# Optimization experiments

Measured on AMD Instinct MI355X. Metric: run time of the kernel, lower is better.

The kernel has to match this reference:

```python
import jax, jax.numpy as jnp
import numpy as np
import math

D_MODEL, D_K, D_V = 1024, 64, 64
B, S = 4, 4096


def setup_inputs() -> dict:
    key = jax.random.key(0)
    ks = jax.random.split(key, 7)
    lim = 1.0 / math.sqrt(D_MODEL)
    return {
        "embeddings": jax.random.normal(ks[0], (B, S, D_MODEL), dtype=jnp.float32),
        "Wq": jax.random.uniform(ks[1], (D_MODEL, D_K), minval=-lim, maxval=lim, dtype=jnp.float32),
        "bq": jax.random.uniform(ks[2], (D_K,), minval=-lim, maxval=lim, dtype=jnp.float32),
        "Wk": jax.random.uniform(ks[3], (D_MODEL, D_K), minval=-lim, maxval=lim, dtype=jnp.float32),
        "bk": jax.random.uniform(ks[4], (D_K,), minval=-lim, maxval=lim, dtype=jnp.float32),
        "Wv": jax.random.uniform(ks[5], (D_MODEL, D_V), minval=-lim, maxval=lim, dtype=jnp.float32),
        "bv": jax.random.uniform(ks[6], (D_V,), minval=-lim, maxval=lim, dtype=jnp.float32),
    }


def reference(embeddings, Wq, bq, Wk, bk, Wv, bv):
    # Q, K: [B, S, d_k]; V: [B, S, d_v]
    Q = embeddings @ Wq + bq
    K = embeddings @ Wk + bk
    V = embeddings @ Wv + bv
    scale = 1.0 / math.sqrt(D_K)
    # scores: [B, S, S]
    scores = jnp.einsum("bsk,btk->bst", Q, K) * scale
    attn = jax.nn.softmax(scores, axis=-1)
    return jnp.einsum("bst,btv->bsv", attn, V)
```

## Files before the change

### kernel.cpp

```cpp
#include <hip/hip_runtime.h>

#define SEQ  4096
#define DMODEL 1024
#define QTOT 16384
#define QSCALE 0.18033688011112042f

typedef __bf16 bf16x8 __attribute__((ext_vector_type(8)));
typedef unsigned short u16x8 __attribute__((ext_vector_type(8)));
typedef float f32x4 __attribute__((ext_vector_type(4)));

static __device__ __forceinline__ unsigned short f2bfbits(float f) {
    unsigned int u = __builtin_bit_cast(unsigned int, f);
    unsigned int lsb = (u >> 16) & 1u;
    u += 0x7fffu + lsb;
    return (unsigned short)(u >> 16);
}

static __device__ __forceinline__ bf16x8 ld_frag(const unsigned short* p) {
    uint4 u = *reinterpret_cast<const uint4*>(p);
    return __builtin_bit_cast(bf16x8, u);
}

__global__ void prep_weights(const float* __restrict__ Wq,
                             const float* __restrict__ Wk,
                             const float* __restrict__ Wv,
                             unsigned short* __restrict__ WtS) {
    int o = blockIdx.x * 256 + threadIdx.x;
    int f = o >> 9, q = o & 511;
    int lane = q >> 3, j = q & 7;
    int kc = f / 12, nt = f - kc * 12;
    int n = nt * 16 + (lane & 15);
    int k = kc * 32 + (lane >> 4) * 8 + j;
    float v;
    if (n < 64)       v = Wq[k * 64 + n];
    else if (n < 128) v = Wk[k * 64 + (n - 64)];
    else              v = Wv[k * 64 + (n - 128)];
    WtS[o] = f2bfbits(v);
}

__global__ __launch_bounds__(256) void proj_cs(
        const float* __restrict__ emb, const unsigned short* __restrict__ WtS,
        const float* __restrict__ bq, const float* __restrict__ bk,
        const float* __restrict__ bv,
        unsigned short* __restrict__ Qb, unsigned short* __restrict__ Kb,
        unsigned short* __restrict__ VT) {
    __shared__ __align__(16) unsigned short Et[2][32 * 256];

    const int tid = threadIdx.x;
    const int w = tid >> 6, lane = tid & 63;
    const int c = lane & 15, qd = lane >> 4;
    const int m = w & 1, nh = w >> 1;
    const int mbase = blockIdx.x * 32;

    f32x4 acc[6];
#pragma unroll
    for (int i = 0; i < 6; i++) acc[i] = (f32x4){0.f, 0.f, 0.f, 0.f};

    const unsigned short* wpB = WtS + nh * 3072 + lane * 8;

    {
        float4 g[8];
#pragma unroll
        for (int rr = 0; rr < 8; rr++)
            g[rr] = *reinterpret_cast<const float4*>(
                emb + (size_t)(mbase + w * 8 + rr) * DMODEL + lane * 4);
#pragma unroll
        for (int rr = 0; rr < 8; rr++) {
            int row = w * 8 + rr;
            ushort4 p;
            p.x = f2bfbits(g[rr].x); p.y = f2bfbits(g[rr].y);
            p.z = f2bfbits(g[rr].z); p.w = f2bfbits(g[rr].w);
            int off = (lane * 8) ^ ((row & 7) << 4);
            *reinterpret_cast<ushort4*>(
                reinterpret_cast<char*>(&Et[0][0]) + row * 512 + off) = p;
        }
    }

    bf16x8 wc[6];
#pragma unroll
    for (int jj = 0; jj < 6; jj++) wc[jj] = ld_frag(wpB + jj * 512);

    __syncthreads();

    int cur = 0;
    for (int mega = 0; mega < 4; mega++) {
        float4 g[8];
        if (mega < 3) {
#pragma unroll
            for (int rr = 0; rr < 8; rr++)
                g[rr] = *reinterpret_cast<const float4*>(
                    emb + (size_t)(mbase + w * 8 + rr) * DMODEL
                        + (mega + 1) * 256 + lane * 4);
        }

        const char* Eb = reinterpret_cast<const char*>(&Et[cur][0]);
        bf16x8 aq[8];
#pragma unroll
        for (int ks = 0; ks < 8; ks++) {
            int off = (ks * 64 + qd * 16) ^ ((c & 7) << 4);
            aq[ks] = ld_frag(reinterpret_cast<const unsigned short*>(
                Eb + (m * 16 + c) * 512 + off));
        }

#pragma unroll
        for (int ks = 0; ks < 8; ks++) {
            int s = mega * 8 + ks;
            bf16x8 wn[6];
            if (s < 31) {
#pragma unroll
                for (int jj = 0; jj < 6; jj++)
                    wn[jj] = ld_frag(wpB + (s + 1) * 6144 + jj * 512);
            } else {
#pragma unroll
                for (int jj = 0; jj < 6; jj++) wn[jj] = wc[jj];
            }
#pragma unroll
            for (int jj = 0; jj < 6; jj++)
                acc[jj] = __builtin_amdgcn_mfma_f32_16x16x32_bf16(aq[ks], wc[jj], acc[jj], 0, 0, 0);
#pragma unroll
            for (int jj = 0; jj < 6; jj++) wc[jj] = wn[jj];
        }

        if (mega < 3) {
#pragma unroll
            for (int rr = 0; rr < 8; rr++) {
                int row = w * 8 + rr;
                ushort4 p;
                p.x = f2bfbits(g[rr].x); p.y = f2bfbits(g[rr].y);
                p.z = f2bfbits(g[rr].z); p.w = f2bfbits(g[rr].w);
                int off = (lane * 8) ^ ((row & 7) << 4);
                *reinterpret_cast<ushort4*>(
                    reinterpret_cast<char*>(&Et[cur ^ 1][0]) + row * 512 + off) = p;
            }
        }
        __syncthreads();
        cur ^= 1;
    }

#pragma unroll
    for (int jj = 0; jj < 6; jj++) {
        int n = (nh * 6 + jj) * 16 + c;
        float bias = (n < 64) ? bq[n] : (n < 128) ? bk[n - 64] : bv[n - 128];
        float fac = (n < 64) ? QSCALE : 1.0f;
#pragma unroll
        for (int r = 0; r < 4; r++) {
            int token = mbase + m * 16 + qd * 4 + r;
            unsigned short bits = f2bfbits((acc[jj][r] + bias) * fac);
            if (n < 64)        Qb[(size_t)token * 64 + n] = bits;
            else if (n < 128)  Kb[(size_t)token * 64 + (n - 64)] = bits;
            else {
                int bb = token >> 12, ss = token & 4095;
                VT[((size_t)bb * 64 + (n - 128)) * SEQ + ss] = bits;
            }
        }
    }
}

__global__ __launch_bounds__(512, 2) void attn(
        const unsigned short* __restrict__ Qb, const unsigned short* __restrict__ Kb,
        const unsigned short* __restrict__ VT,
        float* __restrict__ accP, float* __restrict__ lsumP) {
    __shared__ __align__(16) unsigned short Pl[8][64 * 72];
    __shared__ float l_all[8][64];

    const int tid = threadIdx.x;
    const int w = tid >> 6, lane = tid & 63;
    const int c = lane & 15, qd = lane >> 4;
    const int g3 = blockIdx.x & 7;
    const int b = g3 >> 1;
    const int th = g3 & 1;
    const int qblk = blockIdx.x >> 3;
    const int qbase = qblk * 64;
    const int tstart = th * 2048 + w * 256;

    bf16x8 aq0[4], aq1[4];
#pragma unroll
    for (int qs = 0; qs < 4; qs++) {
        const unsigned short* Qp = Qb + ((size_t)(b << 12) + qbase + qs * 16 + c) * 64 + qd * 8;
        aq0[qs] = ld_frag(Qp);
        aq1[qs] = ld_frag(Qp + 32);
    }

    f32x4 acc[16];
#pragma unroll
    for (int i = 0; i < 16; i++) acc[i] = (f32x4){0.f, 0.f, 0.f, 0.f};
    float lsum[4][4];
#pragma unroll
    for (int qs = 0; qs < 4; qs++)
#pragma unroll
        for (int r = 0; r < 4; r++) lsum[qs][r] = 0.f;

    unsigned short* myP = &Pl[w][0];

#pragma unroll 2
    for (int it = 0; it < 4; it++) {
        const int t0 = tstart + it * 64;
        const unsigned short* Kt = Kb + ((size_t)(b << 12) + t0) * 64;

        bf16x8 bk0[4], bk1[4];
#pragma unroll
        for (int ts = 0; ts < 4; ts++) {
            bk0[ts] = ld_frag(Kt + (ts * 16 + c) * 64 + qd * 8);
            bk1[ts] = ld_frag(Kt + (ts * 16 + c) * 64 + 32 + qd * 8);
        }

#pragma unroll
        for (int qs = 0; qs < 4; qs++) {
            f32x4 sc[4];
#pragma unroll
            for (int ts = 0; ts < 4; ts++) {
                f32x4 z = (f32x4){0.f, 0.f, 0.f, 0.f};
                z = __builtin_amdgcn_mfma_f32_16x16x32_bf16(aq0[qs], bk0[ts], z, 0, 0, 0);
                z = __builtin_amdgcn_mfma_f32_16x16x32_bf16(aq1[qs], bk1[ts], z, 0, 0, 0);
                sc[ts] = z;
            }
#pragma unroll
            for (int ts = 0; ts < 4; ts++)
#pragma unroll
                for (int r = 0; r < 4; r++) {
                    float p = __builtin_amdgcn_exp2f(sc[ts][r]);
                    lsum[qs][r] += p;
                    myP[(qs * 16 + qd * 4 + r) * 72 + ts * 16 + c] = f2bfbits(p);
                }
        }

        bf16x8 bv0[4], bv1[4];
#pragma unroll
        for (int nt = 0; nt < 4; nt++) {
            const unsigned short* Vp = VT + (((size_t)b * 64 + nt * 16 + c) << 12) + t0 + qd * 8;
            bv0[nt] = ld_frag(Vp);
            bv1[nt] = ld_frag(Vp + 32);
        }

#pragma unroll
        for (int qs = 0; qs < 4; qs++) {
            bf16x8 ap0 = ld_frag(&myP[(qs * 16 + c) * 72 + qd * 8]);
            bf16x8 ap1 = ld_frag(&myP[(qs * 16 + c) * 72 + 32 + qd * 8]);
#pragma unroll
            for (int nt = 0; nt < 4; nt++) {
                acc[qs * 4 + nt] = __builtin_amdgcn_mfma_f32_16x16x32_bf16(ap0, bv0[nt], acc[qs * 4 + nt], 0, 0, 0);
                acc[qs * 4 + nt] = __builtin_amdgcn_mfma_f32_16x16x32_bf16(ap1, bv1[nt], acc[qs * 4 + nt], 0, 0, 0);
            }
        }
    }

#pragma unroll
    for (int off = 1; off < 16; off <<= 1)
#pragma unroll
        for (int qs = 0; qs < 4; qs++)
#pragma unroll
            for (int r = 0; r < 4; r++) lsum[qs][r] += __shfl_xor(lsum[qs][r], off);
    if (c == 0) {
#pragma unroll
        for (int qs = 0; qs < 4; qs++)
#pragma unroll
            for (int r = 0; r < 4; r++)
                l_all[w][qs * 16 + qd * 4 + r] = lsum[qs][r];
    }

    float* red = (float*)&Pl[0][0];
    __syncthreads();
    if (w >= 4) {
        float* rp = red + (w - 4) * 4352 + lane * 68;
#pragma unroll
        for (int i = 0; i < 16; i++) *reinterpret_cast<f32x4*>(rp + i * 4) = acc[i];
    }
    __syncthreads();
    if (w < 4) {
        float* rp = red + w * 4352 + lane * 68;
#pragma unroll
        for (int i = 0; i < 16; i++) acc[i] += *reinterpret_cast<const f32x4*>(rp + i * 4);
    }
    __syncthreads();
    if (w == 2 || w == 3) {
        float* rp = red + (w - 2) * 4352 + lane * 68;
#pragma unroll
        for (int i = 0; i < 16; i++) *reinterpret_cast<f32x4*>(rp + i * 4) = acc[i];
    }
    __syncthreads();
    if (w < 2) {
        float* rp = red + w * 4352 + lane * 68;
#pragma unroll
        for (int i = 0; i < 16; i++) acc[i] += *reinterpret_cast<const f32x4*>(rp + i * 4);
    }
    __syncthreads();
    if (w == 1) {
        float* rp = red + lane * 68;
#pragma unroll
        for (int i = 0; i < 16; i++) *reinterpret_cast<f32x4*>(rp + i * 4) = acc[i];
    }
    __syncthreads();
    if (w == 0) {
        float* rp = red + lane * 68;
#pragma unroll
        for (int i = 0; i < 16; i++) acc[i] += *reinterpret_cast<const f32x4*>(rp + i * 4);
        float* accOut = accP + (size_t)th * ((size_t)QTOT * 64);
        float* lOut   = lsumP + (size_t)th * QTOT;
#pragma unroll
        for (int qs = 0; qs < 4; qs++)
#pragma unroll
            for (int r = 0; r < 4; r++) {
                int q = qs * 16 + qd * 4 + r;
                float l = 0.f;
#pragma unroll
                for (int ww = 0; ww < 8; ww++) l += l_all[ww][q];
                size_t row = (size_t)(b << 12) + qbase + q;
                lOut[row] = l;
#pragma unroll
                for (int nt = 0; nt < 4; nt++)
                    accOut[row * 64 + nt * 16 + c] = acc[qs * 4 + nt][r];
            }
    }
}

__global__ __launch_bounds__(256) void finalize(
        const float* __restrict__ accP, const float* __restrict__ lsumP,
        float* __restrict__ out) {
    int idx = blockIdx.x * 256 + threadIdx.x;
    int row = idx >> 4;
    float4 a0 = reinterpret_cast<const float4*>(accP)[idx];
    float4 a1 = reinterpret_cast<const float4*>(accP)[idx + QTOT * 16];
    float inv = 1.0f / (lsumP[row] + lsumP[row + QTOT]);
    float4 o;
    o.x = (a0.x + a1.x) * inv;
    o.y = (a0.y + a1.y) * inv;
    o.z = (a0.z + a1.z) * inv;
    o.w = (a0.w + a1.w) * inv;
    reinterpret_cast<float4*>(out)[idx] = o;
}

extern "C" void kernel_launch(void* const* d_in, const int* in_sizes, int n_in,
                              void* d_out, int out_size, void* d_ws, size_t ws_size,
                              hipStream_t stream) {
    const float* emb = (const float*)d_in[0];
    const float* Wq  = (const float*)d_in[1];
    const float* bq  = (const float*)d_in[2];
    const float* Wk  = (const float*)d_in[3];
    const float* bk  = (const float*)d_in[4];
    const float* Wv  = (const float*)d_in[5];
    const float* bv  = (const float*)d_in[6];
    float* out = (float*)d_out;

    unsigned short* ws = (unsigned short*)d_ws;
    unsigned short* WtS = ws;
    unsigned short* Qb = ws + 192 * 1024;
    unsigned short* Kb = Qb + QTOT * 64;
    unsigned short* VT = Kb + QTOT * 64;
    float* accP  = (float*)(VT + QTOT * 64);
    float* lsumP = accP + (size_t)2 * QTOT * 64;

    prep_weights<<<768, 256, 0, stream>>>(Wq, Wk, Wv, WtS);
    proj_cs<<<512, 256, 0, stream>>>(emb, WtS, bq, bk, bv, Qb, Kb, VT);
    attn<<<512, 512, 0, stream>>>(Qb, Kb, VT, accP, lsumP);
    finalize<<<1024, 256, 0, stream>>>(accP, lsumP, out);
}
```

Baseline: 162.5 us.

## Rewrite attention with 32x32 MFMA and register-resident P via permlane swaps

Replaces the 16x16 MFMA attention kernel with a 32x32x16 MFMA design. Each wave owns 32 queries and computes S^T = K·Q^T, so the exponentiated scores are packed to bf16 with v_cvt_pk_bf16_f32 and rearranged with v_permlane32_swap into the A operand for the PV MFMA, with no LDS staging. Keys are split into four chunks instead of two, which removes the cross-wave LDS reduction and the block barriers; finalize now sums four partials. The cost is more workspace for partial accumulators and heavier reuse of K/V loads from global/L2 across waves.

```diff
diff --git a/kernel.cpp b/kernel.cpp
--- a/kernel.cpp
+++ b/kernel.cpp
@@ -8,6 +8,8 @@
 typedef __bf16 bf16x8 __attribute__((ext_vector_type(8)));
 typedef unsigned short u16x8 __attribute__((ext_vector_type(8)));
 typedef float f32x4 __attribute__((ext_vector_type(4)));
+typedef float f32x16 __attribute__((ext_vector_type(16)));
+typedef unsigned int u32x4 __attribute__((ext_vector_type(4)));
 
 static __device__ __forceinline__ unsigned short f2bfbits(float f) {
     unsigned int u = __builtin_bit_cast(unsigned int, f);
@@ -19,6 +21,12 @@
 static __device__ __forceinline__ bf16x8 ld_frag(const unsigned short* p) {
     uint4 u = *reinterpret_cast<const uint4*>(p);
     return __builtin_bit_cast(bf16x8, u);
+}
+
+static __device__ __forceinline__ unsigned cvtpk(float a, float b) {
+    unsigned r;
+    asm("v_cvt_pk_bf16_f32 %0, %1, %2" : "=v"(r) : "v"(a), "v"(b));
+    return r;
 }
 
 __global__ void prep_weights(const float* __restrict__ Wq,
@@ -156,160 +164,86 @@
     }
 }
 
-__global__ __launch_bounds__(512, 2) void attn(
+__global__ __launch_bounds__(256) void attn32(
         const unsigned short* __restrict__ Qb, const unsigned short* __restrict__ Kb,
         const unsigned short* __restrict__ VT,
         float* __restrict__ accP, float* __restrict__ lsumP) {
-    __shared__ __align__(16) unsigned short Pl[8][64 * 72];
-    __shared__ float l_all[8][64];
-
     const int tid = threadIdx.x;
-    const int w = tid >> 6, lane = tid & 63;
-    const int c = lane & 15, qd = lane >> 4;
-    const int g3 = blockIdx.x & 7;
-    const int b = g3 >> 1;
-    const int th = g3 & 1;
-    const int qblk = blockIdx.x >> 3;
-    const int qbase = qblk * 64;
-    const int tstart = th * 2048 + w * 256;
-
-    bf16x8 aq0[4], aq1[4];
-#pragma unroll
-    for (int qs = 0; qs < 4; qs++) {
-        const unsigned short* Qp = Qb + ((size_t)(b << 12) + qbase + qs * 16 + c) * 64 + qd * 8;
-        aq0[qs] = ld_frag(Qp);
-        aq1[qs] = ld_frag(Qp + 32);
-    }
-
-    f32x4 acc[16];
-#pragma unroll
-    for (int i = 0; i < 16; i++) acc[i] = (f32x4){0.f, 0.f, 0.f, 0.f};
-    float lsum[4][4];
-#pragma unroll
-    for (int qs = 0; qs < 4; qs++)
-#pragma unroll
-        for (int r = 0; r < 4; r++) lsum[qs][r] = 0.f;
-
-    unsigned short* myP = &Pl[w][0];
+    const int w = tid >> 6, l = tid & 63;
+    const int lo = l & 31, hi = l >> 5;
+
+    const int s  = blockIdx.x & 7;
+    const int b  = s >> 1;
+    const int tc = (s & 1) | (((blockIdx.x >> 3) & 1) << 1);
+    const int qi = ((blockIdx.x >> 4) << 2) | w;
+    const int qbase = (b << 12) + qi * 32;
+    const int tbase = tc * 1024;
+
+    const unsigned short* Qp = Qb + (size_t)(qbase + lo) * 64 + hi * 8;
+    bf16x8 qf0 = ld_frag(Qp);
+    bf16x8 qf1 = ld_frag(Qp + 16);
+    bf16x8 qf2 = ld_frag(Qp + 32);
+    bf16x8 qf3 = ld_frag(Qp + 48);
+
+    f32x16 o0 = {}, o1 = {};
+    float lsum = 0.f;
+
+    const unsigned short* KbB = Kb + (size_t)(b << 12) * 64;
+    const unsigned short* VbB = VT + ((size_t)(b * 64) << 12);
 
 #pragma unroll 2
-    for (int it = 0; it < 4; it++) {
-        const int t0 = tstart + it * 64;
-        const unsigned short* Kt = Kb + ((size_t)(b << 12) + t0) * 64;
-
-        bf16x8 bk0[4], bk1[4];
-#pragma unroll
-        for (int ts = 0; ts < 4; ts++) {
-            bk0[ts] = ld_frag(Kt + (ts * 16 + c) * 64 + qd * 8);
-            bk1[ts] = ld_frag(Kt + (ts * 16 + c) * 64 + 32 + qd * 8);
-        }
-
-#pragma unroll
-        for (int qs = 0; qs < 4; qs++) {
-            f32x4 sc[4];
-#pragma unroll
-            for (int ts = 0; ts < 4; ts++) {
-                f32x4 z = (f32x4){0.f, 0.f, 0.f, 0.f};
-                z = __builtin_amdgcn_mfma_f32_16x16x32_bf16(aq0[qs], bk0[ts], z, 0, 0, 0);
-                z = __builtin_amdgcn_mfma_f32_16x16x32_bf16(aq1[qs], bk1[ts], z, 0, 0, 0);
-                sc[ts] = z;
-            }
-#pragma unroll
-            for (int ts = 0; ts < 4; ts++)
-#pragma unroll
-                for (int r = 0; r < 4; r++) {
-                    float p = __builtin_amdgcn_exp2f(sc[ts][r]);
-                    lsum[qs][r] += p;
-                    myP[(qs * 16 + qd * 4 + r) * 72 + ts * 16 + c] = f2bfbits(p);
-                }
-        }
-
-        bf16x8 bv0[4], bv1[4];
-#pragma unroll
-        for (int nt = 0; nt < 4; nt++) {
-            const unsigned short* Vp = VT + (((size_t)b * 64 + nt * 16 + c) << 12) + t0 + qd * 8;
-            bv0[nt] = ld_frag(Vp);
-            bv1[nt] = ld_frag(Vp + 32);
-        }
-
-#pragma unroll
-        for (int qs = 0; qs < 4; qs++) {
-            bf16x8 ap0 = ld_frag(&myP[(qs * 16 + c) * 72 + qd * 8]);
-            bf16x8 ap1 = ld_frag(&myP[(qs * 16 + c) * 72 + 32 + qd * 8]);
-#pragma unroll
-            for (int nt = 0; nt < 4; nt++) {
-                acc[qs * 4 + nt] = __builtin_amdgcn_mfma_f32_16x16x32_bf16(ap0, bv0[nt], acc[qs * 4 + nt], 0, 0, 0);
-                acc[qs * 4 + nt] = __builtin_amdgcn_mfma_f32_16x16x32_bf16(ap1, bv1[nt], acc[qs * 4 + nt], 0, 0, 0);
-            }
-        }
-    }
-
-#pragma unroll
-    for (int off = 1; off < 16; off <<= 1)
-#pragma unroll
-        for (int qs = 0; qs < 4; qs++)
-#pragma unroll
-            for (int r = 0; r < 4; r++) lsum[qs][r] += __shfl_xor(lsum[qs][r], off);
-    if (c == 0) {
-#pragma unroll
-        for (int qs = 0; qs < 4; qs++)
-#pragma unroll
-            for (int r = 0; r < 4; r++)
-                l_all[w][qs * 16 + qd * 4 + r] = lsum[qs][r];
-    }
-
-    float* red = (float*)&Pl[0][0];
-    __syncthreads();
-    if (w >= 4) {
-        float* rp = red + (w - 4) * 4352 + lane * 68;
-#pragma unroll
-        for (int i = 0; i < 16; i++) *reinterpret_cast<f32x4*>(rp + i * 4) = acc[i];
-    }
-    __syncthreads();
-    if (w < 4) {
-        float* rp = red + w * 4352 + lane * 68;
-#pragma unroll
-        for (int i = 0; i < 16; i++) acc[i] += *reinterpret_cast<const f32x4*>(rp + i * 4);
-    }
-    __syncthreads();
-    if (w == 2 || w == 3) {
-        float* rp = red + (w - 2) * 4352 + lane * 68;
-#pragma unroll
-        for (int i = 0; i < 16; i++) *reinterpret_cast<f32x4*>(rp + i * 4) = acc[i];
-    }
-    __syncthreads();
-    if (w < 2) {
-        float* rp = red + w * 4352 + lane * 68;
-#pragma unroll
-        for (int i = 0; i < 16; i++) acc[i] += *reinterpret_cast<const f32x4*>(rp + i * 4);
-    }
-    __syncthreads();
-    if (w == 1) {
-        float* rp = red + lane * 68;
-#pragma unroll
-        for (int i = 0; i < 16; i++) *reinterpret_cast<f32x4*>(rp + i * 4) = acc[i];
-    }
-    __syncthreads();
-    if (w == 0) {
-        float* rp = red + lane * 68;
-#pragma unroll
-        for (int i = 0; i < 16; i++) acc[i] += *reinterpret_cast<const f32x4*>(rp + i * 4);
-        float* accOut = accP + (size_t)th * ((size_t)QTOT * 64);
-        float* lOut   = lsumP + (size_t)th * QTOT;
-#pragma unroll
-        for (int qs = 0; qs < 4; qs++)
-#pragma unroll
-            for (int r = 0; r < 4; r++) {
-                int q = qs * 16 + qd * 4 + r;
-                float l = 0.f;
-#pragma unroll
-                for (int ww = 0; ww < 8; ww++) l += l_all[ww][q];
-                size_t row = (size_t)(b << 12) + qbase + q;
-                lOut[row] = l;
-#pragma unroll
-                for (int nt = 0; nt < 4; nt++)
-                    accOut[row * 64 + nt * 16 + c] = acc[qs * 4 + nt][r];
-            }
+    for (int it = 0; it < 32; ++it) {
+        const int t0 = tbase + it * 32;
+
+        const unsigned short* Kp = KbB + (size_t)(t0 + lo) * 64 + hi * 8;
+        bf16x8 kf0 = ld_frag(Kp);
+        bf16x8 kf1 = ld_frag(Kp + 16);
+        bf16x8 kf2 = ld_frag(Kp + 32);
+        bf16x8 kf3 = ld_frag(Kp + 48);
+        const unsigned short* Vp = VbB + ((size_t)lo << 12) + t0 + hi * 8;
+        bf16x8 vf00 = ld_frag(Vp);
+        bf16x8 vf01 = ld_frag(Vp + 16);
+        bf16x8 vf10 = ld_frag(Vp + (32 << 12));
+        bf16x8 vf11 = ld_frag(Vp + (32 << 12) + 16);
+
+        f32x16 st = {};
+        st = __builtin_amdgcn_mfma_f32_32x32x16_bf16(kf0, qf0, st, 0, 0, 0);
+        st = __builtin_amdgcn_mfma_f32_32x32x16_bf16(kf1, qf1, st, 0, 0, 0);
+        st = __builtin_amdgcn_mfma_f32_32x32x16_bf16(kf2, qf2, st, 0, 0, 0);
+        st = __builtin_amdgcn_mfma_f32_32x32x16_bf16(kf3, qf3, st, 0, 0, 0);
+
+#pragma unroll
+        for (int i = 0; i < 16; i++) {
+            st[i] = __builtin_amdgcn_exp2f(st[i]);
+            lsum += st[i];
+        }
+
+        unsigned a0 = cvtpk(st[0], st[1]),  b0 = cvtpk(st[4], st[5]);
+        unsigned c0 = cvtpk(st[2], st[3]),  d0 = cvtpk(st[6], st[7]);
+        asm("v_permlane32_swap_b32 %0, %1" : "+v"(a0), "+v"(b0));
+        asm("v_permlane32_swap_b32 %0, %1" : "+v"(c0), "+v"(d0));
+        unsigned a1 = cvtpk(st[8],  st[9]),  b1 = cvtpk(st[12], st[13]);
+        unsigned c1 = cvtpk(st[10], st[11]), d1 = cvtpk(st[14], st[15]);
+        asm("v_permlane32_swap_b32 %0, %1" : "+v"(a1), "+v"(b1));
+        asm("v_permlane32_swap_b32 %0, %1" : "+v"(c1), "+v"(d1));
+        bf16x8 pa0 = __builtin_bit_cast(bf16x8, (u32x4){a0, c0, b0, d0});
+        bf16x8 pa1 = __builtin_bit_cast(bf16x8, (u32x4){a1, c1, b1, d1});
+
+        o0 = __builtin_amdgcn_mfma_f32_32x32x16_bf16(pa0, vf00, o0, 0, 0, 0);
+        o0 = __builtin_amdgcn_mfma_f32_32x32x16_bf16(pa1, vf01, o0, 0, 0, 0);
+        o1 = __builtin_amdgcn_mfma_f32_32x32x16_bf16(pa0, vf10, o1, 0, 0, 0);
+        o1 = __builtin_amdgcn_mfma_f32_32x32x16_bf16(pa1, vf11, o1, 0, 0, 0);
+    }
+
+    lsum += __shfl_xor(lsum, 32);
+    if (hi == 0) lsumP[(size_t)tc * QTOT + qbase + lo] = lsum;
+
+    float* accOut = accP + (size_t)tc * ((size_t)QTOT * 64);
+#pragma unroll
+    for (int r = 0; r < 16; r++) {
+        int q = (r & 3) + ((r >> 2) << 3) + (hi << 2);
+        accOut[(size_t)(qbase + q) * 64 + lo]      = o0[r];
+        accOut[(size_t)(qbase + q) * 64 + 32 + lo] = o1[r];
     }
 }
 
@@ -318,14 +252,17 @@
         float* __restrict__ out) {
     int idx = blockIdx.x * 256 + threadIdx.x;
     int row = idx >> 4;
-    float4 a0 = reinterpret_cast<const float4*>(accP)[idx];
-    float4 a1 = reinterpret_cast<const float4*>(accP)[idx + QTOT * 16];
-    float inv = 1.0f / (lsumP[row] + lsumP[row + QTOT]);
+    float4 a = reinterpret_cast<const float4*>(accP)[idx];
+    float lt = lsumP[row];
+#pragma unroll
+    for (int tcq = 1; tcq < 4; tcq++) {
+        float4 ai = reinterpret_cast<const float4*>(accP)[idx + tcq * (QTOT * 16)];
+        a.x += ai.x; a.y += ai.y; a.z += ai.z; a.w += ai.w;
+        lt += lsumP[row + tcq * QTOT];
+    }
+    float inv = 1.0f / lt;
     float4 o;
-    o.x = (a0.x + a1.x) * inv;
-    o.y = (a0.y + a1.y) * inv;
-    o.z = (a0.z + a1.z) * inv;
-    o.w = (a0.w + a1.w) * inv;
+    o.x = a.x * inv; o.y = a.y * inv; o.z = a.z * inv; o.w = a.w * inv;
     reinterpret_cast<float4*>(out)[idx] = o;
 }
 
@@ -347,10 +284,10 @@
     unsigned short* Kb = Qb + QTOT * 64;
     unsigned short* VT = Kb + QTOT * 64;
     float* accP  = (float*)(VT + QTOT * 64);
-    float* lsumP = accP + (size_t)2 * QTOT * 64;
+    float* lsumP = accP + (size_t)4 * QTOT * 64;
 
     prep_weights<<<768, 256, 0, stream>>>(Wq, Wk, Wv, WtS);
     proj_cs<<<512, 256, 0, stream>>>(emb, WtS, bq, bk, bv, Qb, Kb, VT);
-    attn<<<512, 512, 0, stream>>>(Qb, Kb, VT, accP, lsumP);
+    attn32<<<512, 256, 0, stream>>>(Qb, Kb, VT, accP, lsumP);
     finalize<<<1024, 256, 0, stream>>>(accP, lsumP, out);
 }
```

New measurement: 183.0 us. 12.6% more time.
